# Kernel tuning notes

Hardware: AMD Instinct MI355X
Metric: run time of the kernel (lower is better)

The kernel has to match this reference:

```python
import jax, jax.numpy as jnp
import numpy as np

NA = 131072
DG = 150          # GRU hidden size
DS = 50           # static context dim
DIN = 12          # decoding_steps * 2
VEL_CONST = 0.5


def setup_inputs() -> dict:
    key = jax.random.key(0)
    ks = jax.random.split(key, 18)
    s = 0.1  # weight init scale keeps exp(apd_2) numerically tame
    inp = {
        "z": jax.random.normal(ks[0], (NA, 2), jnp.float32),
        "x_flat": jax.random.normal(ks[1], (NA, DIN), jnp.float32),
        "h": jax.random.normal(ks[2], (1, NA, DG), jnp.float32),
        "static": jax.random.normal(ks[3], (NA, DS), jnp.float32),
        "dx": jax.random.normal(ks[4], (NA, 2), jnp.float32),
        "x_prev": jax.random.normal(ks[5], (NA, 2), jnp.float32),
        # GRU params (torch layout: gates ordered r, z, n; shape [3*DG, in])
        "W_ih": jax.random.normal(ks[6], (3 * DG, DIN), jnp.float32) * s,
        "W_hh": jax.random.normal(ks[7], (3 * DG, DG), jnp.float32) * s,
        "b_ih": jax.random.normal(ks[8], (3 * DG,), jnp.float32) * s,
        "b_hh": jax.random.normal(ks[9], (3 * DG,), jnp.float32) * s,
        # MLP: Linear(200,50) -> Softplus -> Linear(50,50) -> Tanh -> Linear(50,6)
        "W1": jax.random.normal(ks[10], (50, DG + DS), jnp.float32) * s,
        "b1": jax.random.normal(ks[11], (50,), jnp.float32) * s,
        "W2": jax.random.normal(ks[12], (50, 50), jnp.float32) * s,
        "b2": jax.random.normal(ks[13], (50,), jnp.float32) * s,
        "W3": jax.random.normal(ks[14], (6, 50), jnp.float32) * s,
        "b3": jax.random.normal(ks[15], (6,), jnp.float32) * s,
    }
    return inp


def _gru_cell(x, h0, W_ih, W_hh, b_ih, b_hh):
    # torch GRU single step. x: [Na, DIN], h0: [Na, DG]
    gx = x @ W_ih.T + b_ih          # [Na, 3*DG]
    gh = h0 @ W_hh.T + b_hh         # [Na, 3*DG]
    xr, xz, xn = jnp.split(gx, 3, axis=-1)
    hr, hz, hn = jnp.split(gh, 3, axis=-1)
    r = jax.nn.sigmoid(xr + hr)
    zg = jax.nn.sigmoid(xz + hz)
    n = jnp.tanh(xn + r * hn)
    return (1.0 - zg) * n + zg * h0


def reference(z, x_flat, h, static, dx, x_prev,
              W_ih, W_hh, b_ih, b_hh, W1, b1, W2, b2, W3, b3):
    h_new = _gru_cell(x_flat, h[0], W_ih, W_hh, b_ih, b_hh)  # [Na, DG]
    dyn_static = jnp.concatenate([h_new, static], axis=-1)    # [Na, DG+DS]
    hmlp = jax.nn.softplus(dyn_static @ W1.T + b1)
    hmlp = jnp.tanh(hmlp @ W2.T + b2)
    out = hmlp @ W3.T + b3                                    # [Na, 6]

    mu_hat = out[:, :2]
    sh = out[:, 2:].reshape(-1, 2, 2)                         # sigma_hat
    mu = x_prev + VEL_CONST * dx + mu_hat

    b = sh[:, 0, 1] + sh[:, 1, 0]
    apd_2 = sh[:, 0, 0] + sh[:, 1, 1]
    amd_2 = sh[:, 0, 0] - sh[:, 1, 1]
    delta = jnp.sqrt(amd_2 ** 2 + b ** 2)
    sinh = jnp.sinh(delta)
    cosh = jnp.cosh(delta)
    tmp1 = sinh / delta
    tmp2 = amd_2 / tmp1
    s00 = cosh + tmp2
    s01 = b * tmp1
    s11 = cosh - tmp2
    sigma = jnp.stack([jnp.stack([s00, s01], axis=-1),
                       jnp.stack([s01, s11], axis=-1)], axis=-2)  # [Na,2,2]
    sigma = sigma * jnp.exp(apd_2)[:, None, None]

    x = jnp.einsum('nij,nj->ni', sigma, z) + mu
    return x, mu, sigma, h_new[None]
```

## Files before the change

kernel.cpp:

```cpp
#include <hip/hip_runtime.h>
#include <math.h>

#define NA 131072
#define NBLK (NA/64)

typedef __bf16 bf16x8 __attribute__((ext_vector_type(8)));
typedef float f32x16 __attribute__((ext_vector_type(16)));

#define APACK_OFF 0
#define BIAS4_OFF 233472
#define W1P_OFF   235904
#define W2P_OFF   262528

__device__ __forceinline__ unsigned short f2b(float f){
  __bf16 h = (__bf16)f;
  unsigned short u;
  __builtin_memcpy(&u, &h, 2);
  return u;
}
__device__ __forceinline__ float b2f(unsigned short u){
  unsigned x = ((unsigned)u) << 16; float f;
  __builtin_memcpy(&f, &x, 4); return f;
}
__device__ __forceinline__ bf16x8 asb(uint4 u){ return __builtin_bit_cast(bf16x8, u); }
__device__ __forceinline__ f32x16 mfma32(bf16x8 a, bf16x8 b, f32x16 c){
  return __builtin_amdgcn_mfma_f32_32x32x16_bf16(a, b, c, 0, 0, 0);
}
__device__ __forceinline__ uint4 packv(const unsigned short* v){
  uint4 p;
  p.x = (unsigned)v[0] | ((unsigned)v[1]<<16);
  p.y = (unsigned)v[2] | ((unsigned)v[3]<<16);
  p.z = (unsigned)v[4] | ((unsigned)v[5]<<16);
  p.w = (unsigned)v[6] | ((unsigned)v[7]<<16);
  return p;
}
__device__ __forceinline__ float fsigmoid(float x){ return 1.f/(1.f+__expf(-x)); }
__device__ __forceinline__ float ftanh(float x){ return 1.f - 2.f/(__expf(2.f*x)+1.f); }

__global__ __launch_bounds__(256) void prep2(
    const float* __restrict__ W_ih, const float* __restrict__ W_hh,
    const float* __restrict__ b_ih, const float* __restrict__ b_hh,
    const float* __restrict__ W1, const float* __restrict__ W2,
    float* __restrict__ ws)
{
  int tid = blockIdx.x*blockDim.x + threadIdx.x;
  int stride = gridDim.x*blockDim.x;
  unsigned short* Ap  = (unsigned short*)((char*)ws + APACK_OFF);
  float*          B4  = (float*)((char*)ws + BIAS4_OFF);
  unsigned short* W1p = (unsigned short*)((char*)ws + W1P_OFF);
  unsigned short* W2p = (unsigned short*)((char*)ws + W2P_OFF);

  for (int s = tid; s < 19*12*64; s += stride){
    int lane = s & 63; int t2 = s >> 6; int ks = t2 % 12; int mt = t2 / 12;
    int R = mt*32 + (lane & 31);
    int kb = ks*16 + (lane >> 5)*8;
    int j = R >> 2, g = R & 3;
    #pragma unroll
    for (int i=0;i<8;i++){
      int k = kb + i; float f = 0.f;
      if (j < 150){
        if (k < 150){
          if (g==0) f = W_hh[j*150+k];
          else if (g==1) f = W_hh[(150+j)*150+k];
          else if (g==2) f = W_hh[(300+j)*150+k];
        } else if (k < 162){
          int kx = k - 150;
          if (g==0) f = W_ih[j*12+kx];
          else if (g==1) f = W_ih[(150+j)*12+kx];
          else if (g==3) f = W_ih[(300+j)*12+kx];
        }
      }
      Ap[s*8+i] = f2b(f);
    }
  }
  for (int j = tid; j < 152; j += stride){
    float4 bv = make_float4(0.f,0.f,0.f,0.f);
    if (j < 150){
      bv.x = b_ih[j]       + b_hh[j];
      bv.y = b_ih[150+j]   + b_hh[150+j];
      bv.z = b_hh[300+j];
      bv.w = b_ih[300+j];
    }
    ((float4*)B4)[j] = bv;
  }
  for (int s = tid; s < 2*13*64; s += stride){
    int lane = s & 63; int t2 = s >> 6; int ks = t2 % 13; int mt = t2 / 13;
    int o = mt*32 + (lane & 31);
    int kb = ks*16 + (lane >> 5)*8;
    #pragma unroll
    for (int i=0;i<8;i++){
      int k = kb + i;
      float f = (o < 50 && k < 200) ? W1[o*200+k] : 0.f;
      W1p[s*8+i] = f2b(f);
    }
  }
  for (int s = tid; s < 2*4*64; s += stride){
    int lane = s & 63; int t2 = s >> 6; int ks = t2 % 4; int mt = t2 / 4;
    int o = mt*32 + (lane & 31);
    int kb = ks*16 + (lane >> 5)*8;
    #pragma unroll
    for (int i=0;i<8;i++){
      int k = kb + i;
      float f = (o < 50 && k < 50) ? W2[o*50+k] : 0.f;
      W2p[s*8+i] = f2b(f);
    }
  }
}

__global__ __launch_bounds__(256,3) void fused_kernel(
    const float* __restrict__ x_flat, const float* __restrict__ h_in,
    const float* __restrict__ st, const float* __restrict__ z_in,
    const float* __restrict__ dx, const float* __restrict__ xp,
    const float* __restrict__ b1, const float* __restrict__ b2,
    const float* __restrict__ W3, const float* __restrict__ b3,
    const unsigned short* __restrict__ Apack, const float* __restrict__ Bias4,
    const unsigned short* __restrict__ W1p, const unsigned short* __restrict__ W2p,
    float* __restrict__ out)
{
  __shared__ unsigned short sm_ag[64*216];
  __shared__ float          sm_x[64*13];
  __shared__ unsigned short sm_h1[64*72];
  __shared__ float          sm_h2[64*51];

  int t = threadIdx.x; int lane = t & 63; int w = t >> 6;
  int hi = lane >> 5, cl = lane & 31;
  long ab = (long)blockIdx.x * 64;
  unsigned* ag32 = (unsigned*)sm_ag;

  for (int s = t; s < 64*36; s += 256) ((unsigned*)sm_h1)[s] = 0u;
  const float2* h2p = (const float2*)h_in;
  for (int s = t; s < 4800; s += 256){
    int a = s/75, k2 = s - a*75;
    float2 v = h2p[ab*75 + s];
    ag32[a*108 + k2] = (unsigned)f2b(v.x) | ((unsigned)f2b(v.y) << 16);
  }
  const float2* s2p = (const float2*)st;
  for (int s = t; s < 1600; s += 256){
    int a = s/25, k2 = s - a*25;
    float2 v = s2p[ab*25 + s];
    ag32[a*108 + 75 + k2] = (unsigned)f2b(v.x) | ((unsigned)f2b(v.y) << 16);
  }
  for (int s = t; s < 512; s += 256)
    ag32[(s>>3)*108 + 100 + (s&7)] = 0u;
  for (int s = t; s < 768; s += 256){
    int a = s/12, k = s - a*12;
    sm_x[a*13 + k] = x_flat[ab*12 + s];
  }
  __syncthreads();

  bf16x8 B0[11], B1[11];
  {
    const uint4* r0 = (const uint4*)(sm_ag + cl*216);
    const uint4* r1 = (const uint4*)(sm_ag + (32+cl)*216);
    #pragma unroll
    for (int ks=0; ks<9; ks++){
      B0[ks] = asb(r0[ks*2+hi]);
      B1[ks] = asb(r1[ks*2+hi]);
    }
    #pragma unroll
    for (int ks=9; ks<11; ks++){
      unsigned short v0[8], v1[8];
      #pragma unroll
      for (int i=0;i<8;i++){
        int k = ks*16 + hi*8 + i;
        unsigned short e0=0, e1=0;
        if (k < 150){ e0 = sm_ag[cl*216+k]; e1 = sm_ag[(32+cl)*216+k]; }
        else if (k < 162){
          e0 = f2b(sm_x[cl*13 + (k-150)]);
          e1 = f2b(sm_x[(32+cl)*13 + (k-150)]);
        }
        v0[i]=e0; v1[i]=e1;
      }
      B0[ks] = asb(packv(v0)); B1[ks] = asb(packv(v1));
    }
  }
  __syncthreads();

  const uint4* ApV = (const uint4*)Apack;
  #pragma unroll 1
  for (int mt = w; mt < 19; mt += 4){
    f32x16 acc0;
    #pragma unroll
    for (int q=0;q<4;q++){
      float4 bq = ((const float4*)Bias4)[mt*8 + 2*q + hi];
      acc0[4*q+0]=bq.x; acc0[4*q+1]=bq.y; acc0[4*q+2]=bq.z; acc0[4*q+3]=bq.w;
    }
    f32x16 acc1 = acc0;
    const uint4* ap = ApV + (size_t)(mt*12)*64 + lane;
    #pragma unroll
    for (int ks=0; ks<11; ks++){
      bf16x8 af = asb(ap[ks*64]);
      acc0 = mfma32(af, B0[ks], acc0);
      acc1 = mfma32(af, B1[ks], acc1);
    }
    #pragma unroll
    for (int nt=0; nt<2; nt++){
      const f32x16& acc = nt ? acc1 : acc0;
      int a = nt*32 + cl;
      #pragma unroll
      for (int q=0;q<4;q++){
        int j = mt*8 + 2*q + hi;
        if (j < 150){
          float h0 = b2f(sm_ag[a*216 + j]);
          float r = fsigmoid(acc[4*q+0]);
          float z = fsigmoid(acc[4*q+1]);
          float n = ftanh(acc[4*q+3] + r*acc[4*q+2]);
          sm_ag[a*216 + j] = f2b(n + z*(h0 - n));
        }
      }
    }
  }
  __syncthreads();

  float2* oh2 = (float2*)(out + (size_t)8*NA);
  for (int s = t; s < 4800; s += 256){
    int a = s/75, k2 = s - a*75;
    unsigned u = ag32[a*108 + k2];
    float2 v; v.x = b2f((unsigned short)u); v.y = b2f((unsigned short)(u>>16));
    oh2[ab*75 + s] = v;
  }

  int mt2 = w >> 1; int a2 = (w & 1)*32 + cl;
  f32x16 acc;
  #pragma unroll
  for (int r=0;r<16;r++){
    int o = mt2*32 + (r&3) + 8*(r>>2) + 4*hi;
    acc[r] = (o < 50) ? b1[o] : 0.f;
  }
  {
    const uint4* rv  = (const uint4*)(sm_ag + a2*216);
    const uint4* w1v = (const uint4*)W1p;
    #pragma unroll
    for (int ks=0; ks<13; ks++){
      acc = mfma32(asb(w1v[(mt2*13+ks)*64 + lane]), asb(rv[ks*2+hi]), acc);
    }
  }
  #pragma unroll
  for (int r=0;r<16;r++){
    int o = mt2*32 + (r&3) + 8*(r>>2) + 4*hi;
    if (o < 50){
      float xx = acc[r];
      float spv = fmaxf(xx,0.f) + __logf(1.f + __expf(-fabsf(xx)));
      sm_h1[a2*72 + o] = f2b(spv);
    }
  }
  __syncthreads();

  f32x16 acc2;
  #pragma unroll
  for (int r=0;r<16;r++){
    int o = mt2*32 + (r&3) + 8*(r>>2) + 4*hi;
    acc2[r] = (o < 50) ? b2[o] : 0.f;
  }
  {
    const uint4* r1v = (const uint4*)(sm_h1 + a2*72);
    const uint4* w2v = (const uint4*)W2p;
    #pragma unroll
    for (int ks=0; ks<4; ks++){
      acc2 = mfma32(asb(w2v[(mt2*4+ks)*64 + lane]), asb(r1v[ks*2+hi]), acc2);
    }
  }
  #pragma unroll
  for (int r=0;r<16;r++){
    int o = mt2*32 + (r&3) + 8*(r>>2) + 4*hi;
    if (o < 50) sm_h2[a2*51 + o] = ftanh(acc2[r]);
  }
  __syncthreads();

  if (t < 64){
    int a = t; long ga = ab + a;
    float o6[6];
    #pragma unroll
    for (int jj=0;jj<6;jj++) o6[jj] = b3[jj];
    for (int k=0;k<50;k++){
      float v = sm_h2[a*51 + k];
      #pragma unroll
      for (int jj=0;jj<6;jj++) o6[jj] = fmaf(v, W3[jj*50+k], o6[jj]);
    }
    float mu0 = xp[ga*2+0] + 0.5f*dx[ga*2+0] + o6[0];
    float mu1 = xp[ga*2+1] + 0.5f*dx[ga*2+1] + o6[1];
    float bb  = o6[3] + o6[4];
    float apd = o6[2] + o6[5];
    float amd = o6[2] - o6[5];
    float delta = sqrtf(amd*amd + bb*bb);
    float e  = __expf(delta);
    float ei = 1.f/e;
    float sinh_ = 0.5f*(e - ei);
    float cosh_ = 0.5f*(e + ei);
    float tmp1 = sinh_/delta;
    float tmp2 = amd/tmp1;
    float ea = __expf(apd);
    float s00 = (cosh_+tmp2)*ea;
    float s01 = (bb*tmp1)*ea;
    float s11 = (cosh_-tmp2)*ea;
    float z0 = z_in[ga*2+0], z1 = z_in[ga*2+1];
    out[ga*2+0] = s00*z0 + s01*z1 + mu0;
    out[ga*2+1] = s01*z0 + s11*z1 + mu1;
    out[(size_t)2*NA + ga*2+0] = mu0;
    out[(size_t)2*NA + ga*2+1] = mu1;
    out[(size_t)4*NA + ga*4+0] = s00;
    out[(size_t)4*NA + ga*4+1] = s01;
    out[(size_t)4*NA + ga*4+2] = s01;
    out[(size_t)4*NA + ga*4+3] = s11;
  }
}

extern "C" void kernel_launch(void* const* d_in, const int* in_sizes, int n_in,
                              void* d_out, int out_size, void* d_ws, size_t ws_size,
                              hipStream_t stream) {
  const float* z      = (const float*)d_in[0];
  const float* x_flat = (const float*)d_in[1];
  const float* h      = (const float*)d_in[2];
  const float* st     = (const float*)d_in[3];
  const float* dx     = (const float*)d_in[4];
  const float* xp     = (const float*)d_in[5];
  const float* W_ih   = (const float*)d_in[6];
  const float* W_hh   = (const float*)d_in[7];
  const float* b_ih   = (const float*)d_in[8];
  const float* b_hh   = (const float*)d_in[9];
  const float* W1     = (const float*)d_in[10];
  const float* b1     = (const float*)d_in[11];
  const float* W2     = (const float*)d_in[12];
  const float* b2     = (const float*)d_in[13];
  const float* W3     = (const float*)d_in[14];
  const float* b3     = (const float*)d_in[15];
  float* out = (float*)d_out;
  float* ws  = (float*)d_ws;

  const unsigned short* Apack = (const unsigned short*)((char*)ws + APACK_OFF);
  const float*          Bias4 = (const float*)((char*)ws + BIAS4_OFF);
  const unsigned short* W1p   = (const unsigned short*)((char*)ws + W1P_OFF);
  const unsigned short* W2p   = (const unsigned short*)((char*)ws + W2P_OFF);

  hipLaunchKernelGGL(prep2, dim3(128), dim3(256), 0, stream,
                     W_ih, W_hh, b_ih, b_hh, W1, W2, ws);
  hipLaunchKernelGGL(fused_kernel, dim3(NBLK), dim3(256), 0, stream,
                     x_flat, h, st, z, dx, xp, b1, b2, W3, b3,
                     Apack, Bias4, W1p, W2p, out);
}
```

Before: 115.1 us.

## Reorder GRU K layout to put x first and alias shared memory buffers

```diff
diff --git a/kernel.cpp b/kernel.cpp
--- a/kernel.cpp
+++ b/kernel.cpp
@@ -8,9 +8,9 @@
 typedef float f32x16 __attribute__((ext_vector_type(16)));
 
 #define APACK_OFF 0
-#define BIAS4_OFF 233472
-#define W1P_OFF   235904
-#define W2P_OFF   262528
+#define BIAS4_OFF 214016
+#define W1P_OFF   216448
+#define W2P_OFF   243072
 
 __device__ __forceinline__ unsigned short f2b(float f){
   __bf16 h = (__bf16)f;
@@ -25,14 +25,6 @@
 __device__ __forceinline__ bf16x8 asb(uint4 u){ return __builtin_bit_cast(bf16x8, u); }
 __device__ __forceinline__ f32x16 mfma32(bf16x8 a, bf16x8 b, f32x16 c){
   return __builtin_amdgcn_mfma_f32_32x32x16_bf16(a, b, c, 0, 0, 0);
-}
-__device__ __forceinline__ uint4 packv(const unsigned short* v){
-  uint4 p;
-  p.x = (unsigned)v[0] | ((unsigned)v[1]<<16);
-  p.y = (unsigned)v[2] | ((unsigned)v[3]<<16);
-  p.z = (unsigned)v[4] | ((unsigned)v[5]<<16);
-  p.w = (unsigned)v[6] | ((unsigned)v[7]<<16);
-  return p;
 }
 __device__ __forceinline__ float fsigmoid(float x){ return 1.f/(1.f+__expf(-x)); }
 __device__ __forceinline__ float ftanh(float x){ return 1.f - 2.f/(__expf(2.f*x)+1.f); }
@@ -50,8 +42,8 @@
   unsigned short* W1p = (unsigned short*)((char*)ws + W1P_OFF);
   unsigned short* W2p = (unsigned short*)((char*)ws + W2P_OFF);
 
-  for (int s = tid; s < 19*12*64; s += stride){
-    int lane = s & 63; int t2 = s >> 6; int ks = t2 % 12; int mt = t2 / 12;
+  for (int s = tid; s < 19*11*64; s += stride){
+    int lane = s & 63; int t2 = s >> 6; int ks = t2 % 11; int mt = t2 / 11;
     int R = mt*32 + (lane & 31);
     int kb = ks*16 + (lane >> 5)*8;
     int j = R >> 2, g = R & 3;
@@ -59,15 +51,15 @@
     for (int i=0;i<8;i++){
       int k = kb + i; float f = 0.f;
       if (j < 150){
-        if (k < 150){
-          if (g==0) f = W_hh[j*150+k];
-          else if (g==1) f = W_hh[(150+j)*150+k];
-          else if (g==2) f = W_hh[(300+j)*150+k];
-        } else if (k < 162){
-          int kx = k - 150;
-          if (g==0) f = W_ih[j*12+kx];
-          else if (g==1) f = W_ih[(150+j)*12+kx];
-          else if (g==3) f = W_ih[(300+j)*12+kx];
+        if (k < 12){
+          if (g==0) f = W_ih[j*12+k];
+          else if (g==1) f = W_ih[(150+j)*12+k];
+          else if (g==3) f = W_ih[(300+j)*12+k];
+        } else if (k >= 16 && k < 166){
+          int kh = k - 16;
+          if (g==0) f = W_hh[j*150+kh];
+          else if (g==1) f = W_hh[(150+j)*150+kh];
+          else if (g==2) f = W_hh[(300+j)*150+kh];
         }
       }
       Ap[s*8+i] = f2b(f);
@@ -107,7 +99,7 @@
   }
 }
 
-__global__ __launch_bounds__(256,3) void fused_kernel(
+__global__ __launch_bounds__(256,4) void fused_kernel(
     const float* __restrict__ x_flat, const float* __restrict__ h_in,
     const float* __restrict__ st, const float* __restrict__ z_in,
     const float* __restrict__ dx, const float* __restrict__ xp,
@@ -117,17 +109,17 @@
     const unsigned short* __restrict__ W1p, const unsigned short* __restrict__ W2p,
     float* __restrict__ out)
 {
-  __shared__ unsigned short sm_ag[64*216];
-  __shared__ float          sm_x[64*13];
-  __shared__ unsigned short sm_h1[64*72];
-  __shared__ float          sm_h2[64*51];
+  __shared__ char smem[36864];
+  unsigned short* sm_ag = (unsigned short*)smem;
+  unsigned short* sm_xf = (unsigned short*)(smem + 27648);
+  unsigned short* sm_h1 = (unsigned short*)(smem + 27648);
+  float*          sm_h2 = (float*)smem;
+  unsigned*       ag32  = (unsigned*)sm_ag;
 
   int t = threadIdx.x; int lane = t & 63; int w = t >> 6;
   int hi = lane >> 5, cl = lane & 31;
   long ab = (long)blockIdx.x * 64;
-  unsigned* ag32 = (unsigned*)sm_ag;
-
-  for (int s = t; s < 64*36; s += 256) ((unsigned*)sm_h1)[s] = 0u;
+
   const float2* h2p = (const float2*)h_in;
   for (int s = t; s < 4800; s += 256){
     int a = s/75, k2 = s - a*75;
@@ -142,39 +134,31 @@
   }
   for (int s = t; s < 512; s += 256)
     ag32[(s>>3)*108 + 100 + (s&7)] = 0u;
-  for (int s = t; s < 768; s += 256){
-    int a = s/12, k = s - a*12;
-    sm_x[a*13 + k] = x_flat[ab*12 + s];
+  for (int s = t; s < 1024; s += 256){
+    int nt2 = s >> 9; int r = s & 511; int ln = r >> 3; int i = r & 7;
+    int k = ((ln >> 5) << 3) + i;
+    int agent = nt2*32 + (ln & 31);
+    unsigned short v = 0;
+    if (k < 12) v = f2b(x_flat[(ab+agent)*12 + k]);
+    sm_xf[s] = v;
   }
   __syncthreads();
 
   bf16x8 B0[11], B1[11];
   {
+    B0[0] = asb(((const uint4*)sm_xf)[lane]);
+    B1[0] = asb(((const uint4*)sm_xf)[64 + lane]);
     const uint4* r0 = (const uint4*)(sm_ag + cl*216);
     const uint4* r1 = (const uint4*)(sm_ag + (32+cl)*216);
     #pragma unroll
-    for (int ks=0; ks<9; ks++){
-      B0[ks] = asb(r0[ks*2+hi]);
-      B1[ks] = asb(r1[ks*2+hi]);
-    }
-    #pragma unroll
-    for (int ks=9; ks<11; ks++){
-      unsigned short v0[8], v1[8];
-      #pragma unroll
-      for (int i=0;i<8;i++){
-        int k = ks*16 + hi*8 + i;
-        unsigned short e0=0, e1=0;
-        if (k < 150){ e0 = sm_ag[cl*216+k]; e1 = sm_ag[(32+cl)*216+k]; }
-        else if (k < 162){
-          e0 = f2b(sm_x[cl*13 + (k-150)]);
-          e1 = f2b(sm_x[(32+cl)*13 + (k-150)]);
-        }
-        v0[i]=e0; v1[i]=e1;
-      }
-      B0[ks] = asb(packv(v0)); B1[ks] = asb(packv(v1));
-    }
-  }
-  __syncthreads();
+    for (int ks=1; ks<11; ks++){
+      B0[ks] = asb(r0[(ks-1)*2 + hi]);
+      B1[ks] = asb(r1[(ks-1)*2 + hi]);
+    }
+  }
+  __syncthreads();
+
+  for (int s = t; s < 2304; s += 256) ((unsigned*)sm_h1)[s] = 0u;
 
   const uint4* ApV = (const uint4*)Apack;
   #pragma unroll 1
@@ -186,7 +170,7 @@
       acc0[4*q+0]=bq.x; acc0[4*q+1]=bq.y; acc0[4*q+2]=bq.z; acc0[4*q+3]=bq.w;
     }
     f32x16 acc1 = acc0;
-    const uint4* ap = ApV + (size_t)(mt*12)*64 + lane;
+    const uint4* ap = ApV + (size_t)(mt*11)*64 + lane;
     #pragma unroll
     for (int ks=0; ks<11; ks++){
       bf16x8 af = asb(ap[ks*64]);
```

After: 123.3 us. 1.07x slower.
